# Performance work log

Measured on AMD Instinct MI355X. Metric: run time of the kernel, lower is better.

The kernel has to match this reference:

```python
import jax, jax.numpy as jnp
import numpy as np

B, N, D_IN, D_OUT = 4, 2048, 4096, 4096
E, R, D_ATT = 8, 16, 128
SCALING = 16.0 / 16.0  # alpha / rank


def setup_inputs() -> dict:
    key = jax.random.key(0)
    ks = jax.random.split(key, 8)
    x = jax.random.normal(ks[0], (B, N, D_IN), dtype=jnp.float32)
    weight = jax.random.normal(ks[1], (D_OUT, D_IN), dtype=jnp.float32) * 0.02  # frozen base
    bias = jax.random.normal(ks[2], (D_OUT,), dtype=jnp.float32) * 0.02
    router_V = jax.random.normal(ks[3], (D_ATT, D_IN), dtype=jnp.float32) * 0.02
    router_U = jax.random.normal(ks[4], (D_ATT, D_IN), dtype=jnp.float32) * 0.02
    router_W = jax.random.normal(ks[5], (E, D_ATT), dtype=jnp.float32) * 0.02
    experts_A = jax.random.normal(ks[6], (E, D_IN, R), dtype=jnp.float32) * 0.01
    experts_B = jax.random.normal(ks[7], (E, R, D_OUT), dtype=jnp.float32) * 0.01
    return {"x": x, "weight": weight, "bias": bias, "router_V": router_V,
            "router_U": router_U, "router_W": router_W,
            "experts_A": experts_A, "experts_B": experts_B}


def reference(x, weight, bias, router_V, router_U, router_W, experts_A, experts_B):
    # Frozen base projection: F.linear(x, weight, bias)
    base = jnp.einsum('bnd,od->bno', x, weight) + bias
    # ABMIL gated-attention router
    v = jnp.tanh(jnp.einsum('bnd,ad->bna', x, router_V))            # [B,N,D_att]
    u = jax.nn.sigmoid(jnp.einsum('bnd,ad->bna', x, router_U))      # [B,N,D_att]
    scores = jnp.einsum('bna,ea->bne', v * u, router_W)             # [B,N,E]
    router_weights = jax.nn.sigmoid(scores)                         # independent sigmoid gates
    # Per-expert low-rank path (dropout is identity at inference / p=0)
    lora_down = jnp.einsum('bnd,edr->bner', x, experts_A)           # [B,N,E,R]
    weighted = lora_down * router_weights[..., None]
    moe_out = jnp.einsum('bner,erd->bnd', weighted, experts_B)      # [B,N,D_out]
    return base + SCALING * moe_out
```

## Files before the change

### kernel.cpp

```cpp
#include <hip/hip_runtime.h>
#include <hip/hip_bf16.h>

#define M_TOT   8192
#define D_IN    4096
#define D_OUT   4096
#define N_E     8
#define N_R     16
#define D_ATT   128
#define ER      128
#define CATN    384
#define KEXT    4224
#define NTK     66
#define NX4     (8388608L)
#define NW4     (4194304L)

typedef __attribute__((ext_vector_type(8)))  __bf16 bf16x8;
typedef __attribute__((ext_vector_type(4)))  float  f32x4;

__device__ __forceinline__ ushort f2bf(float f) {
  union { float f; unsigned u; } v; v.f = f;
  unsigned r = (v.u + 0x7fffu + ((v.u >> 16) & 1u)) >> 16;
  return (ushort)r;
}
__device__ __forceinline__ float bf2f(ushort u) {
  union { unsigned u; float f; } v; v.u = ((unsigned)u) << 16;
  return v.f;
}

__global__ void conv_xw_kernel(const float* __restrict__ x, const float* __restrict__ w,
                               ushort* __restrict__ xe, ushort* __restrict__ we) {
  long i = blockIdx.x * (long)blockDim.x + threadIdx.x;
  const float* src; ushort* dst; long j;
  if (i < NX4) { src = x; dst = xe; j = i; }
  else         { src = w; dst = we; j = i - NX4; }
  const float4 a = reinterpret_cast<const float4*>(src)[j];
  ushort4 r; r.x = f2bf(a.x); r.y = f2bf(a.y); r.z = f2bf(a.z); r.w = f2bf(a.w);
  long row = j >> 10, c4 = (j & 1023) << 2;
  *reinterpret_cast<ushort4*>(dst + row * KEXT + c4) = r;
}

__global__ void prep_small_kernel(const float* __restrict__ rV, const float* __restrict__ rU,
                                  const float* __restrict__ expA, const float* __restrict__ expB,
                                  ushort* __restrict__ cat, ushort* __restrict__ we) {
  int b = blockIdx.x;
  if (b < 1024) {
    const float* src = (b < 512) ? rV : rU;
    ushort* dst = cat + ((b < 512) ? 0 : (size_t)D_ATT * D_IN);
    int i = (b & 511) * 256 + threadIdx.x;
    const float4 a = reinterpret_cast<const float4*>(src)[i];
    ushort4 r; r.x = f2bf(a.x); r.y = f2bf(a.y); r.z = f2bf(a.z); r.w = f2bf(a.w);
    reinterpret_cast<ushort4*>(dst)[i] = r;
  } else if (b < 3072) {
    int idx = (b - 1024) * 256 + threadIdx.x;
    int j = idx >> 12, d = idx & 4095;
    int e = j >> 4, r = j & 15;
    cat[(size_t)(2 * D_ATT + j) * D_IN + d] = f2bf(expA[((size_t)e * D_IN + d) * N_R + r]);
  } else {
    int idx = (b - 3072) * 256 + threadIdx.x;
    int j = idx >> 12, o = idx & 4095;
    we[(size_t)o * KEXT + D_IN + j] = f2bf(expB[(size_t)j * D_OUT + o]);
  }
}

__global__ void gate_kernel(const ushort* __restrict__ P, const float* __restrict__ rW,
                            ushort* __restrict__ wtd) {
  int token = blockIdx.x * 4 + (threadIdx.x >> 6);
  int l = threadIdx.x & 63;
  const ushort* p0 = P + (size_t)token * CATN;
  const ushort* p1 = p0 + (size_t)M_TOT * CATN;
  float v0 = tanhf(bf2f(p0[l])      + bf2f(p1[l]));
  float v1 = tanhf(bf2f(p0[l + 64]) + bf2f(p1[l + 64]));
  float u0 = 1.f / (1.f + __expf(-(bf2f(p0[D_ATT + l])      + bf2f(p1[D_ATT + l]))));
  float u1 = 1.f / (1.f + __expf(-(bf2f(p0[D_ATT + l + 64]) + bf2f(p1[D_ATT + l + 64]))));
  float g0 = v0 * u0, g1 = v1 * u1;
  float rw[8];
  #pragma unroll
  for (int e = 0; e < 8; ++e) {
    float s = g0 * rW[e * D_ATT + l] + g1 * rW[e * D_ATT + l + 64];
    #pragma unroll
    for (int off = 32; off > 0; off >>= 1) s += __shfl_xor(s, off);
    rw[e] = 1.f / (1.f + __expf(-s));
  }
  int q = l >> 4;
  float rw_a = (q == 0) ? rw[0] : (q == 1) ? rw[1] : (q == 2) ? rw[2] : rw[3];
  float rw_b = (q == 0) ? rw[4] : (q == 1) ? rw[5] : (q == 2) ? rw[6] : rw[7];
  float lo_a = bf2f(p0[2 * D_ATT + l])      + bf2f(p1[2 * D_ATT + l]);
  float lo_b = bf2f(p0[2 * D_ATT + l + 64]) + bf2f(p1[2 * D_ATT + l + 64]);
  wtd[(size_t)token * KEXT + l]      = f2bf(lo_a * rw_a);
  wtd[(size_t)token * KEXT + l + 64] = f2bf(lo_b * rw_b);
}

__global__ __launch_bounds__(256, 4)
void gemm128_kernel(const ushort* __restrict__ A, const ushort* __restrict__ Bm,
                    ushort* __restrict__ C)
{
  __shared__ ushort As[128 * 64];
  __shared__ ushort Bs[128 * 64];
  const int tid = threadIdx.x;
  const int w = tid >> 6, l = tid & 63;
  const int wr = w >> 1, wc = w & 1;
  const int l16 = l & 15, lq = l >> 4;
  const int brow = blockIdx.y * 128;
  const int bcol = blockIdx.x * 128;
  const int kt0 = (int)blockIdx.z << 5;

  f32x4 acc[4][4] = {};

  for (int kt = kt0; kt < kt0 + 32; ++kt) {
    int k0 = kt << 6;
    #pragma unroll
    for (int c = 0; c < 4; ++c) {
      int rloc = w * 32 + c * 8;
      int rl = rloc + (l >> 3);
      int kk = k0 + (l & 7) * 8;
      const ushort* ga = A  + (size_t)(brow + rl) * KEXT + kk;
      const ushort* gb = Bm + (size_t)(bcol + rl) * D_IN + kk;
      __builtin_amdgcn_global_load_lds((const __attribute__((address_space(1))) void*)ga,
                                       (__attribute__((address_space(3))) void*)(As + rloc * 64),
                                       16, 0, 0);
      __builtin_amdgcn_global_load_lds((const __attribute__((address_space(1))) void*)gb,
                                       (__attribute__((address_space(3))) void*)(Bs + rloc * 64),
                                       16, 0, 0);
    }
    __syncthreads();

    #pragma unroll
    for (int ks = 0; ks < 2; ++ks) {
      bf16x8 af[4], bfv[4];
      #pragma unroll
      for (int mi = 0; mi < 4; ++mi)
        af[mi] = *reinterpret_cast<const bf16x8*>(As + (wr * 64 + mi * 16 + l16) * 64 + ks * 32 + lq * 8);
      #pragma unroll
      for (int ni = 0; ni < 4; ++ni)
        bfv[ni] = *reinterpret_cast<const bf16x8*>(Bs + (wc * 64 + ni * 16 + l16) * 64 + ks * 32 + lq * 8);
      #pragma unroll
      for (int mi = 0; mi < 4; ++mi)
        #pragma unroll
        for (int ni = 0; ni < 4; ++ni)
          acc[mi][ni] = __builtin_amdgcn_mfma_f32_16x16x32_bf16(af[mi], bfv[ni], acc[mi][ni], 0, 0, 0);
    }
    __syncthreads();
  }

  ushort* Cz = C + (size_t)blockIdx.z * M_TOT * CATN;
  #pragma unroll
  for (int ni = 0; ni < 4; ++ni) {
    int col = bcol + wc * 64 + ni * 16 + l16;
    #pragma unroll
    for (int mi = 0; mi < 4; ++mi) {
      f32x4 v = acc[mi][ni];
      int row0 = brow + wr * 64 + mi * 16 + lq * 4;
      #pragma unroll
      for (int j = 0; j < 4; ++j)
        Cz[(size_t)(row0 + j) * CATN + col] = f2bf(v[j]);
    }
  }
}

__global__ __launch_bounds__(512, 2)
void gemm256_kernel(const ushort* __restrict__ A, const ushort* __restrict__ Bm,
                    float* __restrict__ C, const float* __restrict__ bias)
{
  __shared__ ushort lds[2][2][2][8192];
  const int tid = threadIdx.x;
  const int wid = tid >> 6, l = tid & 63;
  const int wr = wid >> 2, wc = wid & 3;
  const int l16 = l & 15, lq = l >> 4;
  const int rxor = (l16 & 7) << 3;

  const int xcd = (int)blockIdx.x & 7, q = (int)blockIdx.x >> 3;
  const int brow = ((xcd >> 1) * 8 + (q >> 3)) * 256;
  const int bcol = ((xcd & 1) * 8 + (q & 7)) * 256;

  const int srow = tid >> 3;
  const int scol = (((tid & 7) ^ ((tid >> 3) & 7)) << 3);

#define STAGE(buf_, mat_, half_, kt_) do {                                        \
    const ushort* _s = (mat_) ? Bm : A;                                           \
    int _rb = ((mat_) ? bcol : brow) + (half_) * 128 + srow;                      \
    ushort* _d = &lds[(buf_)][(mat_)][(half_)][wid * 512];                        \
    _Pragma("unroll")                                                             \
    for (int _c = 0; _c < 2; ++_c) {                                              \
      const ushort* _g = _s + (size_t)(_rb + _c * 64) * KEXT + (kt_) * 64 + scol; \
      __builtin_amdgcn_global_load_lds(                                           \
          (const __attribute__((address_space(1))) void*)_g,                      \
          (__attribute__((address_space(3))) void*)(_d + _c * 4096), 16, 0, 0);   \
    } } while (0)

#define LDA_FRAG(buf_, mi_, ks_) \
  (*reinterpret_cast<const bf16x8*>(&lds[(buf_)][0][wr][((mi_) * 16 + l16) * 64 + (((ks_) * 32 + lq * 8) ^ rxor)]))
#define LDB_FRAG(buf_, ni_, ks_) \
  (*reinterpret_cast<const bf16x8*>(&lds[(buf_)][1][wc >> 1][((wc & 1) * 64 + (ni_) * 16 + l16) * 64 + (((ks_) * 32 + lq * 8) ^ rxor)]))

#define RD_ALO(buf_, dst_) \
    _Pragma("unroll") for (int mi = 0; mi < 4; ++mi) \
      _Pragma("unroll") for (int ks = 0; ks < 2; ++ks) dst_[mi][ks] = LDA_FRAG(buf_, mi, ks);
#define RD_BLO(buf_, dst_) \
    _Pragma("unroll") for (int ni = 0; ni < 2; ++ni) \
      _Pragma("unroll") for (int ks = 0; ks < 2; ++ks) dst_[ni][ks] = LDB_FRAG(buf_, ni, ks);

#define MFMA_Q(accm0_, accn0_, a_, b_) \
    _Pragma("unroll") for (int mi = 0; mi < 4; ++mi) \
      _Pragma("unroll") for (int ni = 0; ni < 2; ++ni) \
        _Pragma("unroll") for (int ks = 0; ks < 2; ++ks) \
          acc[(accm0_) + mi][(accn0_) + ni] = __builtin_amdgcn_mfma_f32_16x16x32_bf16( \
              a_[mi][ks], b_[ni][ks], acc[(accm0_) + mi][(accn0_) + ni], 0, 0, 0);

#define TILE(t_, buf_, aIn_, b0In_, aOut_, b0Out_) do {                           \
    bf16x8 b1[2][2], aHi[4][2];                                                   \
    const int ktA = ((t_) + 1 < NTK) ? (t_) + 1 : NTK - 1;                        \
    const int ktB = ((t_) + 2 < NTK) ? (t_) + 2 : NTK - 1;                        \
                                                                          \
    STAGE(buf_ ^ 1, 0, 0, ktA);                                                   \
    __builtin_amdgcn_s_barrier();                                                 \
    asm volatile("s_waitcnt lgkmcnt(0)" ::: "memory");                            \
    __builtin_amdgcn_s_setprio(1);                                                \
    _Pragma("unroll") for (int ni = 0; ni < 2; ++ni)                              \
      _Pragma("unroll") for (int ks = 0; ks < 2; ++ks)                            \
        b1[ni][ks] = LDB_FRAG(buf_, ni + 2, ks);                                  \
    MFMA_Q(0, 0, aIn_, b0In_);                                                    \
    __builtin_amdgcn_s_setprio(0);                                                \
    __builtin_amdgcn_s_barrier();                                                 \
                                                                          \
    STAGE(buf_ ^ 1, 0, 1, ktA);                                                   \
    __builtin_amdgcn_s_barrier();                                                 \
    asm volatile("s_waitcnt lgkmcnt(0)" ::: "memory");                            \
    __builtin_amdgcn_s_setprio(1);                                                \
    _Pragma("unroll") for (int mi = 0; mi < 4; ++mi)                              \
      _Pragma("unroll") for (int ks = 0; ks < 2; ++ks)                            \
        aHi[mi][ks] = LDA_FRAG(buf_, mi + 4, ks);                                 \
    MFMA_Q(0, 2, aIn_, b1);                                                       \
    __builtin_amdgcn_s_setprio(0);                                                \
    __builtin_amdgcn_s_barrier();                                                 \
                                                                          \
    STAGE(buf_, 1, 0, ktB);                                                       \
    __builtin_amdgcn_s_barrier();                                                 \
    asm volatile("s_waitcnt lgkmcnt(0)" ::: "memory");                            \
    __builtin_amdgcn_s_setprio(1);                                                \
    MFMA_Q(4, 2, aHi, b1);                                                        \
    __builtin_amdgcn_s_setprio(0);                                                \
    __builtin_amdgcn_s_barrier();                                                 \
                                                                          \
    STAGE(buf_, 1, 1, ktB);                                                       \
    asm volatile("s_waitcnt vmcnt(4)" ::: "memory");                              \
    __builtin_amdgcn_s_barrier();                                                 \
    __builtin_amdgcn_s_setprio(1);                                                \
    RD_ALO(buf_ ^ 1, aOut_);                                                      \
    RD_BLO(buf_ ^ 1, b0Out_);                                                     \
    MFMA_Q(4, 0, aHi, b0In_);                                                     \
    __builtin_amdgcn_s_setprio(0);                                                \
    __builtin_amdgcn_s_barrier();                                                 \
  } while (0)

  f32x4 acc[8][4] = {};
  bf16x8 aA[4][2], b0A[2][2], aB[4][2], b0B[2][2];

  STAGE(0, 0, 0, 0); STAGE(0, 0, 1, 0);
  STAGE(0, 1, 0, 0); STAGE(0, 1, 1, 0);
  STAGE(1, 1, 0, 1); STAGE(1, 1, 1, 1);
  asm volatile("s_waitcnt vmcnt(4)" ::: "memory");
  __builtin_amdgcn_s_barrier();
  RD_ALO(0, aA);
  RD_BLO(0, b0A);

  #pragma unroll 1
  for (int tp = 0; tp < NTK / 2; ++tp) {
    TILE(2 * tp,     0, aA, b0A, aB, b0B);
    TILE(2 * tp + 1, 1, aB, b0B, aA, b0A);
  }

  asm volatile("s_waitcnt vmcnt(0) lgkmcnt(0)" ::: "memory");

  #pragma unroll
  for (int ni = 0; ni < 4; ++ni) {
    int col = bcol + wc * 64 + ni * 16 + l16;
    float bs = bias[col];
    #pragma unroll
    for (int mi = 0; mi < 8; ++mi) {
      int row0 = brow + wr * 128 + mi * 16 + lq * 4;
      #pragma unroll
      for (int j = 0; j < 4; ++j)
        C[(size_t)(row0 + j) * D_OUT + col] = acc[mi][ni][j] + bs;
    }
  }
#undef STAGE
#undef LDA_FRAG
#undef LDB_FRAG
#undef RD_ALO
#undef RD_BLO
#undef MFMA_Q
#undef TILE
}

extern "C" void kernel_launch(void* const* d_in, const int* in_sizes, int n_in,
                              void* d_out, int out_size, void* d_ws, size_t ws_size,
                              hipStream_t stream) {
  const float* x      = (const float*)d_in[0];
  const float* weight = (const float*)d_in[1];
  const float* bias   = (const float*)d_in[2];
  const float* rV     = (const float*)d_in[3];
  const float* rU     = (const float*)d_in[4];
  const float* rW     = (const float*)d_in[5];
  const float* expA   = (const float*)d_in[6];
  const float* expB   = (const float*)d_in[7];
  float* out = (float*)d_out;

  ushort* xe  = (ushort*)d_ws;
  ushort* we  = xe  + (size_t)M_TOT * KEXT;
  ushort* cat = we  + (size_t)D_OUT * KEXT;
  ushort* P   = cat + (size_t)CATN * D_IN;

  conv_xw_kernel<<<dim3((NX4 + NW4) / 256), 256, 0, stream>>>(x, weight, xe, we);

  prep_small_kernel<<<dim3(5120), 256, 0, stream>>>(rV, rU, expA, expB, cat, we);

  gemm128_kernel<<<dim3(CATN / 128, M_TOT / 128, 2), 256, 0, stream>>>(xe, cat, P);

  gate_kernel<<<dim3(M_TOT / 4), 256, 0, stream>>>(P, rW, xe + D_IN);

  gemm256_kernel<<<dim3((D_OUT / 256) * (M_TOT / 256)), 512, 0, stream>>>(xe, we, out, bias);
}
```

Measured before the change: 341.1 us.

## Fuse x fp32-to-bf16 conversion into router GEMM and merge prep kernels

The router/LoRA-down GEMM now reads x in fp32 directly, converts it to bf16 in registers, and writes it into LDS. Blocks with blockIdx.x==0 also write the converted tile to the extended x buffer for the main GEMM. This removes the separate pass over x and folds the weight conversion into the small-prep kernel, saving one launch and one full read/write of x. The cost is that the gemm128 A loads become synchronous register loads instead of direct-to-LDS loads, and the launch bound is lowered to 3 blocks per SM.

```diff
diff --git a/kernel.cpp b/kernel.cpp
--- a/kernel.cpp
+++ b/kernel.cpp
@@ -11,7 +11,6 @@
 #define CATN    384
 #define KEXT    4224
 #define NTK     66
-#define NX4     (8388608L)
 #define NW4     (4194304L)
 
 typedef __attribute__((ext_vector_type(8)))  __bf16 bf16x8;
@@ -26,37 +25,38 @@
   union { unsigned u; float f; } v; v.u = ((unsigned)u) << 16;
   return v.f;
 }
-
-__global__ void conv_xw_kernel(const float* __restrict__ x, const float* __restrict__ w,
-                               ushort* __restrict__ xe, ushort* __restrict__ we) {
-  long i = blockIdx.x * (long)blockDim.x + threadIdx.x;
-  const float* src; ushort* dst; long j;
-  if (i < NX4) { src = x; dst = xe; j = i; }
-  else         { src = w; dst = we; j = i - NX4; }
-  const float4 a = reinterpret_cast<const float4*>(src)[j];
-  ushort4 r; r.x = f2bf(a.x); r.y = f2bf(a.y); r.z = f2bf(a.z); r.w = f2bf(a.w);
-  long row = j >> 10, c4 = (j & 1023) << 2;
-  *reinterpret_cast<ushort4*>(dst + row * KEXT + c4) = r;
-}
-
-__global__ void prep_small_kernel(const float* __restrict__ rV, const float* __restrict__ rU,
-                                  const float* __restrict__ expA, const float* __restrict__ expB,
-                                  ushort* __restrict__ cat, ushort* __restrict__ we) {
+__device__ __forceinline__ unsigned cvt_pk(float lo, float hi) {
+  unsigned r;
+  asm("v_cvt_pk_bf16_f32 %0, %1, %2" : "=v"(r) : "v"(lo), "v"(hi));
+  return r;
+}
+
+__global__ void prep_all_kernel(const float* __restrict__ wgt,
+                                const float* __restrict__ rV, const float* __restrict__ rU,
+                                const float* __restrict__ expA, const float* __restrict__ expB,
+                                ushort* __restrict__ we, ushort* __restrict__ cat) {
   int b = blockIdx.x;
-  if (b < 1024) {
-    const float* src = (b < 512) ? rV : rU;
-    ushort* dst = cat + ((b < 512) ? 0 : (size_t)D_ATT * D_IN);
-    int i = (b & 511) * 256 + threadIdx.x;
+  if (b < 16384) {
+    long j = (long)b * 256 + threadIdx.x;
+    const float4 a = reinterpret_cast<const float4*>(wgt)[j];
+    ushort4 r; r.x = f2bf(a.x); r.y = f2bf(a.y); r.z = f2bf(a.z); r.w = f2bf(a.w);
+    long row = j >> 10, c4 = (j & 1023) << 2;
+    *reinterpret_cast<ushort4*>(we + row * KEXT + c4) = r;
+  } else if (b < 17408) {
+    int bb = b - 16384;
+    const float* src = (bb < 512) ? rV : rU;
+    ushort* dst = cat + ((bb < 512) ? 0 : (size_t)D_ATT * D_IN);
+    int i = (bb & 511) * 256 + threadIdx.x;
     const float4 a = reinterpret_cast<const float4*>(src)[i];
     ushort4 r; r.x = f2bf(a.x); r.y = f2bf(a.y); r.z = f2bf(a.z); r.w = f2bf(a.w);
     reinterpret_cast<ushort4*>(dst)[i] = r;
-  } else if (b < 3072) {
-    int idx = (b - 1024) * 256 + threadIdx.x;
+  } else if (b < 19456) {
+    int idx = (b - 17408) * 256 + threadIdx.x;
     int j = idx >> 12, d = idx & 4095;
     int e = j >> 4, r = j & 15;
     cat[(size_t)(2 * D_ATT + j) * D_IN + d] = f2bf(expA[((size_t)e * D_IN + d) * N_R + r]);
   } else {
-    int idx = (b - 3072) * 256 + threadIdx.x;
+    int idx = (b - 19456) * 256 + threadIdx.x;
     int j = idx >> 12, o = idx & 4095;
     we[(size_t)o * KEXT + D_IN + j] = f2bf(expB[(size_t)j * D_OUT + o]);
   }
@@ -90,9 +90,9 @@
   wtd[(size_t)token * KEXT + l + 64] = f2bf(lo_b * rw_b);
 }
 
-__global__ __launch_bounds__(256, 4)
-void gemm128_kernel(const ushort* __restrict__ A, const ushort* __restrict__ Bm,
-                    ushort* __restrict__ C)
+__global__ __launch_bounds__(256, 3)
+void gemm128_kernel(const float* __restrict__ X, const ushort* __restrict__ Bm,
+                    ushort* __restrict__ C, ushort* __restrict__ xe)
 {
   __shared__ ushort As[128 * 64];
   __shared__ ushort Bs[128 * 64];
@@ -103,6 +103,7 @@
   const int brow = blockIdx.y * 128;
   const int bcol = blockIdx.x * 128;
   const int kt0 = (int)blockIdx.z << 5;
+  const bool side = (blockIdx.x == 0);
 
   f32x4 acc[4][4] = {};
 
@@ -113,11 +114,16 @@
       int rloc = w * 32 + c * 8;
       int rl = rloc + (l >> 3);
       int kk = k0 + (l & 7) * 8;
-      const ushort* ga = A  + (size_t)(brow + rl) * KEXT + kk;
+      const float* gx = X + (size_t)(brow + rl) * D_IN + kk;
+      float4 a0 = *reinterpret_cast<const float4*>(gx);
+      float4 a1 = *reinterpret_cast<const float4*>(gx + 4);
+      uint4 pk;
+      pk.x = cvt_pk(a0.x, a0.y); pk.y = cvt_pk(a0.z, a0.w);
+      pk.z = cvt_pk(a1.x, a1.y); pk.w = cvt_pk(a1.z, a1.w);
+      *reinterpret_cast<uint4*>(As + (size_t)rl * 64 + (l & 7) * 8) = pk;
+      if (side)
+        *reinterpret_cast<uint4*>(xe + (size_t)(brow + rl) * KEXT + kk) = pk;
       const ushort* gb = Bm + (size_t)(bcol + rl) * D_IN + kk;
-      __builtin_amdgcn_global_load_lds((const __attribute__((address_space(1))) void*)ga,
-                                       (__attribute__((address_space(3))) void*)(As + rloc * 64),
-                                       16, 0, 0);
       __builtin_amdgcn_global_load_lds((const __attribute__((address_space(1))) void*)gb,
                                        (__attribute__((address_space(3))) void*)(Bs + rloc * 64),
                                        16, 0, 0);
@@ -310,11 +316,10 @@
   ushort* cat = we  + (size_t)D_OUT * KEXT;
   ushort* P   = cat + (size_t)CATN * D_IN;
 
-  conv_xw_kernel<<<dim3((NX4 + NW4) / 256), 256, 0, stream>>>(x, weight, xe, we);
-
-  prep_small_kernel<<<dim3(5120), 256, 0, stream>>>(rV, rU, expA, expB, cat, we);
-
-  gemm128_kernel<<<dim3(CATN / 128, M_TOT / 128, 2), 256, 0, stream>>>(xe, cat, P);
+  prep_all_kernel<<<dim3(16384 + 1024 + 2048 + 2048), 256, 0, stream>>>(
+      weight, rV, rU, expA, expB, we, cat);
+
+  gemm128_kernel<<<dim3(CATN / 128, M_TOT / 128, 2), 256, 0, stream>>>(x, cat, P, xe);
 
   gate_kernel<<<dim3(M_TOT / 4), 256, 0, stream>>>(P, rW, xe + D_IN);
 
```

After: 396.9 us. 1.16x slower.

## Restructure main GEMM tile loop into two phases with full B fragment prefetch

Applied to the files above, without the earlier changes.

The 256x256 GEMM's per-k-tile schedule goes from four phases, each with its own barrier, to two. Each phase now issues two LDS stage loads and then runs 32 MFMAs over half the M rows with all four N fragments. The B fragments are prefetched whole for the next tile, which needs more registers, so launch bounds drop from 2 to 1 block per CU. This halves the barriers and raises MFMA work per sync, at the cost of lower occupancy and less interleaving of global loads with compute.

```diff
diff --git a/kernel.cpp b/kernel.cpp
--- a/kernel.cpp
+++ b/kernel.cpp
@@ -157,7 +157,7 @@
   }
 }
 
-__global__ __launch_bounds__(512, 2)
+__global__ __launch_bounds__(512, 1)
 void gemm256_kernel(const ushort* __restrict__ A, const ushort* __restrict__ Bm,
                     float* __restrict__ C, const float* __restrict__ bias)
 {
@@ -195,65 +195,50 @@
 #define RD_ALO(buf_, dst_) \
     _Pragma("unroll") for (int mi = 0; mi < 4; ++mi) \
       _Pragma("unroll") for (int ks = 0; ks < 2; ++ks) dst_[mi][ks] = LDA_FRAG(buf_, mi, ks);
-#define RD_BLO(buf_, dst_) \
-    _Pragma("unroll") for (int ni = 0; ni < 2; ++ni) \
+#define RD_AHI(buf_, dst_) \
+    _Pragma("unroll") for (int mi = 0; mi < 4; ++mi) \
+      _Pragma("unroll") for (int ks = 0; ks < 2; ++ks) dst_[mi][ks] = LDA_FRAG(buf_, mi + 4, ks);
+#define RD_BALL(buf_, dst_) \
+    _Pragma("unroll") for (int ni = 0; ni < 4; ++ni) \
       _Pragma("unroll") for (int ks = 0; ks < 2; ++ks) dst_[ni][ks] = LDB_FRAG(buf_, ni, ks);
 
-#define MFMA_Q(accm0_, accn0_, a_, b_) \
+#define MFMA_H(accm0_, a_, b_) \
     _Pragma("unroll") for (int mi = 0; mi < 4; ++mi) \
-      _Pragma("unroll") for (int ni = 0; ni < 2; ++ni) \
+      _Pragma("unroll") for (int ni = 0; ni < 4; ++ni) \
         _Pragma("unroll") for (int ks = 0; ks < 2; ++ks) \
-          acc[(accm0_) + mi][(accn0_) + ni] = __builtin_amdgcn_mfma_f32_16x16x32_bf16( \
-              a_[mi][ks], b_[ni][ks], acc[(accm0_) + mi][(accn0_) + ni], 0, 0, 0);
-
-#define TILE(t_, buf_, aIn_, b0In_, aOut_, b0Out_) do {                           \
-    bf16x8 b1[2][2], aHi[4][2];                                                   \
+          acc[(accm0_) + mi][ni] = __builtin_amdgcn_mfma_f32_16x16x32_bf16( \
+              a_[mi][ks], b_[ni][ks], acc[(accm0_) + mi][ni], 0, 0, 0);
+
+#define TILE2(t_, buf_, aIn_, bIn_, aOut_, bOut_) do {                            \
+    bf16x8 aHi[4][2];                                                             \
     const int ktA = ((t_) + 1 < NTK) ? (t_) + 1 : NTK - 1;                        \
     const int ktB = ((t_) + 2 < NTK) ? (t_) + 2 : NTK - 1;                        \
                                                                           \
     STAGE(buf_ ^ 1, 0, 0, ktA);                                                   \
-    __builtin_amdgcn_s_barrier();                                                 \
-    asm volatile("s_waitcnt lgkmcnt(0)" ::: "memory");                            \
-    __builtin_amdgcn_s_setprio(1);                                                \
-    _Pragma("unroll") for (int ni = 0; ni < 2; ++ni)                              \
-      _Pragma("unroll") for (int ks = 0; ks < 2; ++ks)                            \
-        b1[ni][ks] = LDB_FRAG(buf_, ni + 2, ks);                                  \
-    MFMA_Q(0, 0, aIn_, b0In_);                                                    \
-    __builtin_amdgcn_s_setprio(0);                                                \
-    __builtin_amdgcn_s_barrier();                                                 \
-                                                                          \
     STAGE(buf_ ^ 1, 0, 1, ktA);                                                   \
     __builtin_amdgcn_s_barrier();                                                 \
     asm volatile("s_waitcnt lgkmcnt(0)" ::: "memory");                            \
     __builtin_amdgcn_s_setprio(1);                                                \
-    _Pragma("unroll") for (int mi = 0; mi < 4; ++mi)                              \
-      _Pragma("unroll") for (int ks = 0; ks < 2; ++ks)                            \
-        aHi[mi][ks] = LDA_FRAG(buf_, mi + 4, ks);                                 \
-    MFMA_Q(0, 2, aIn_, b1);                                                       \
+    RD_AHI(buf_, aHi);                                                            \
+    MFMA_H(0, aIn_, bIn_);                                                        \
     __builtin_amdgcn_s_setprio(0);                                                \
     __builtin_amdgcn_s_barrier();                                                 \
                                                                           \
     STAGE(buf_, 1, 0, ktB);                                                       \
+    STAGE(buf_, 1, 1, ktB);                                                       \
+    asm volatile("s_waitcnt vmcnt(4)" ::: "memory");                              \
     __builtin_amdgcn_s_barrier();                                                 \
     asm volatile("s_waitcnt lgkmcnt(0)" ::: "memory");                            \
     __builtin_amdgcn_s_setprio(1);                                                \
-    MFMA_Q(4, 2, aHi, b1);                                                        \
-    __builtin_amdgcn_s_setprio(0);                                                \
-    __builtin_amdgcn_s_barrier();                                                 \
-                                                                          \
-    STAGE(buf_, 1, 1, ktB);                                                       \
-    asm volatile("s_waitcnt vmcnt(4)" ::: "memory");                              \
-    __builtin_amdgcn_s_barrier();                                                 \
-    __builtin_amdgcn_s_setprio(1);                                                \
     RD_ALO(buf_ ^ 1, aOut_);                                                      \
-    RD_BLO(buf_ ^ 1, b0Out_);                                                     \
-    MFMA_Q(4, 0, aHi, b0In_);                                                     \
+    RD_BALL(buf_ ^ 1, bOut_);                                                     \
+    MFMA_H(4, aHi, bIn_);                                                         \
     __builtin_amdgcn_s_setprio(0);                                                \
     __builtin_amdgcn_s_barrier();                                                 \
   } while (0)
 
   f32x4 acc[8][4] = {};
-  bf16x8 aA[4][2], b0A[2][2], aB[4][2], b0B[2][2];
+  bf16x8 aA[4][2], bA[4][2], aB[4][2], bB[4][2];
 
   STAGE(0, 0, 0, 0); STAGE(0, 0, 1, 0);
   STAGE(0, 1, 0, 0); STAGE(0, 1, 1, 0);
@@ -261,12 +246,12 @@
   asm volatile("s_waitcnt vmcnt(4)" ::: "memory");
   __builtin_amdgcn_s_barrier();
   RD_ALO(0, aA);
-  RD_BLO(0, b0A);
+  RD_BALL(0, bA);
 
   #pragma unroll 1
   for (int tp = 0; tp < NTK / 2; ++tp) {
-    TILE(2 * tp,     0, aA, b0A, aB, b0B);
-    TILE(2 * tp + 1, 1, aB, b0B, aA, b0A);
+    TILE2(2 * tp,     0, aA, bA, aB, bB);
+    TILE2(2 * tp + 1, 1, aB, bB, aA, bA);
   }
 
   asm volatile("s_waitcnt vmcnt(0) lgkmcnt(0)" ::: "memory");
@@ -287,9 +272,10 @@
 #undef LDA_FRAG
 #undef LDB_FRAG
 #undef RD_ALO
-#undef RD_BLO
-#undef MFMA_Q
-#undef TILE
+#undef RD_AHI
+#undef RD_BALL
+#undef MFMA_H
+#undef TILE2
 }
 
 extern "C" void kernel_launch(void* const* d_in, const int* in_sizes, int n_in,
```

Result: slower. 348.3 us (+2.1%).
